# Performance work log

Hardware: AMD Instinct MI355X
Metric: run time of the kernel (lower is better)

The kernel has to match this reference:

```python
import jax, jax.numpy as jnp
import numpy as np

FILLER = 10.1  # filler_value from __init__
B, C, L, KEEP = 128, 16, 16384, 12288


def setup_inputs() -> dict:
    key = jax.random.key(0)
    k1, k2, k3, k4 = jax.random.split(key, 4)
    x1 = jax.random.normal(k1, (B, C, 4096), dtype=jnp.float32)
    x2 = jax.random.normal(k2, (B, C, 4096), dtype=jnp.float32)
    x3 = jax.random.normal(k3, (B, C, L), dtype=jnp.float32)
    # Scatter exactly (L - KEEP) filler entries at random positions in every row,
    # so per-row compaction yields a uniform length KEEP (required by np.stack
    # in the original module).
    u = jax.random.uniform(k4, (B, C, L))
    ranks = jnp.argsort(jnp.argsort(u, axis=-1), axis=-1)  # random permutation ranks
    fill_mask = ranks < (L - KEEP)
    x3 = jnp.where(fill_mask, jnp.float32(FILLER), x3)
    return {"x1": x1, "x2": x2, "x3": x3, "keep_len": KEEP}


def reference(x1, x2, x3, keep_len):
    # Per-row stream compaction: drop entries equal to FILLER, keep original
    # order of survivors, output fixed length keep_len.
    is_filler = x3 == jnp.float32(FILLER)          # [B, C, L] bool
    # Stable argsort moves non-filler (False=0) to the front, order-preserving.
    order = jnp.argsort(is_filler, axis=-1, stable=True)  # [B, C, L]
    compacted = jnp.take_along_axis(x3, order, axis=-1)    # [B, C, L]
    return compacted[..., :keep_len]                        # [B, C, keep_len]
```

## Files before the change

kernel.cpp:

```cpp
#include <hip/hip_runtime.h>


#define FILLER_VAL 10.1f
constexpr int L_LEN = 16384;
constexpr int KEEP_LEN = 12288;
constexpr int BLOCK = 256;
constexpr int CHUNK = BLOCK * 4;

__global__ __launch_bounds__(BLOCK) void compact_rows_kernel(
    const float* __restrict__ x3, float* __restrict__ out)
{
    const int row = blockIdx.x;
    const float* __restrict__ in = x3 + (size_t)row * L_LEN;
    float* __restrict__ o = out + (size_t)row * KEEP_LEN;

    const int tid  = threadIdx.x;
    const int lane = tid & 63;
    const int wid  = tid >> 6;

    __shared__ int wave_tot[BLOCK / 64];

    const unsigned long long lt_mask = (1ULL << lane) - 1ULL;

    int base = 0;

    #pragma unroll 1
    for (int chunk = 0; chunk < L_LEN; chunk += CHUNK) {
        float4 v = *reinterpret_cast<const float4*>(in + chunk + tid * 4);

        const bool p0 = v.x != FILLER_VAL;
        const bool p1 = v.y != FILLER_VAL;
        const bool p2 = v.z != FILLER_VAL;
        const bool p3 = v.w != FILLER_VAL;

        const unsigned long long m0 = __ballot(p0);
        const unsigned long long m1 = __ballot(p1);
        const unsigned long long m2 = __ballot(p2);
        const unsigned long long m3 = __ballot(p3);

        const int before = __popcll(m0 & lt_mask) + __popcll(m1 & lt_mask)
                         + __popcll(m2 & lt_mask) + __popcll(m3 & lt_mask);
        const int wtot   = __popcll(m0) + __popcll(m1) + __popcll(m2) + __popcll(m3);

        if (lane == 0) wave_tot[wid] = wtot;
        __syncthreads();

        int wave_base = 0;
        #pragma unroll
        for (int w = 0; w < BLOCK / 64; ++w) {
            if (w < wid) wave_base += wave_tot[w];
        }
        int chunk_total = 0;
        #pragma unroll
        for (int w = 0; w < BLOCK / 64; ++w) chunk_total += wave_tot[w];

        int pos = base + wave_base + before;

        if (p0) { if (pos < KEEP_LEN) o[pos] = v.x; ++pos; }
        if (p1) { if (pos < KEEP_LEN) o[pos] = v.y; ++pos; }
        if (p2) { if (pos < KEEP_LEN) o[pos] = v.z; ++pos; }
        if (p3) { if (pos < KEEP_LEN) o[pos] = v.w; ++pos; }

        base += chunk_total;
        __syncthreads();
    }
}

extern "C" void kernel_launch(void* const* d_in, const int* in_sizes, int n_in,
                              void* d_out, int out_size, void* d_ws, size_t ws_size,
                              hipStream_t stream)
{
    const float* x3 = (const float*)d_in[2];
    float* out = (float*)d_out;

    const int rows = in_sizes[2] / L_LEN;

    compact_rows_kernel<<<rows, BLOCK, 0, stream>>>(x3, out);
}
```

Before: 262.0 us.

## Load whole row into registers upfront and batch wave-count syncs per half

The loop of sixteen chunks, each with its own global load and two barriers, is replaced by issuing all sixteen float4 loads per thread up front, held in two register arrays of eight chunks. Ballots and wave totals are computed for eight chunks at a time and stored in a shared table, so a whole half needs only one barrier. This targets load latency and barrier stalls in a kernel that runs one block per row. In exchange, register use per thread rises sharply, which may lower occupancy.

```diff
diff --git a/kernel.cpp b/kernel.cpp
--- a/kernel.cpp
+++ b/kernel.cpp
@@ -2,10 +2,12 @@
 
 
 #define FILLER_VAL 10.1f
-constexpr int L_LEN = 16384;
+constexpr int L_LEN   = 16384;
 constexpr int KEEP_LEN = 12288;
-constexpr int BLOCK = 256;
-constexpr int CHUNK = BLOCK * 4;
+constexpr int BLOCK   = 256;
+constexpr int NW      = BLOCK / 64;
+constexpr int CHUNK   = BLOCK * 4;
+constexpr int HC      = 8;
 
 __global__ __launch_bounds__(BLOCK) void compact_rows_kernel(
     const float* __restrict__ x3, float* __restrict__ out)
@@ -17,52 +19,81 @@
     const int tid  = threadIdx.x;
     const int lane = tid & 63;
     const int wid  = tid >> 6;
+    const unsigned long long lt = (1ULL << lane) - 1ULL;
 
-    __shared__ int wave_tot[BLOCK / 64];
+    __shared__ int wtot[2][HC][NW];
 
-    const unsigned long long lt_mask = (1ULL << lane) - 1ULL;
+    float4 va[HC], vb[HC];
+    #pragma unroll
+    for (int c = 0; c < HC; ++c)
+        va[c] = *reinterpret_cast<const float4*>(in + c * CHUNK + tid * 4);
+    #pragma unroll
+    for (int c = 0; c < HC; ++c)
+        vb[c] = *reinterpret_cast<const float4*>(in + (HC + c) * CHUNK + tid * 4);
 
-    int base = 0;
+    int before_a[HC];
+    #pragma unroll
+    for (int c = 0; c < HC; ++c) {
+        unsigned long long m0 = __ballot(va[c].x != FILLER_VAL);
+        unsigned long long m1 = __ballot(va[c].y != FILLER_VAL);
+        unsigned long long m2 = __ballot(va[c].z != FILLER_VAL);
+        unsigned long long m3 = __ballot(va[c].w != FILLER_VAL);
+        before_a[c] = __popcll(m0 & lt) + __popcll(m1 & lt)
+                    + __popcll(m2 & lt) + __popcll(m3 & lt);
+        if (lane == 0)
+            wtot[0][c][wid] = __popcll(m0) + __popcll(m1)
+                            + __popcll(m2) + __popcll(m3);
+    }
+    __syncthreads();
 
-    #pragma unroll 1
-    for (int chunk = 0; chunk < L_LEN; chunk += CHUNK) {
-        float4 v = *reinterpret_cast<const float4*>(in + chunk + tid * 4);
+    int run = 0;
+    #pragma unroll
+    for (int c = 0; c < HC; ++c) {
+        int wb = run;
+        #pragma unroll
+        for (int w = 0; w < NW; ++w) {
+            int t = wtot[0][c][w];
+            if (w < wid) wb += t;
+            run += t;
+        }
+        int pos = wb + before_a[c];
+        float4 v = va[c];
+        if (v.x != FILLER_VAL) { if (pos < KEEP_LEN) o[pos] = v.x; ++pos; }
+        if (v.y != FILLER_VAL) { if (pos < KEEP_LEN) o[pos] = v.y; ++pos; }
+        if (v.z != FILLER_VAL) { if (pos < KEEP_LEN) o[pos] = v.z; ++pos; }
+        if (v.w != FILLER_VAL) { if (pos < KEEP_LEN) o[pos] = v.w; ++pos; }
+    }
 
-        const bool p0 = v.x != FILLER_VAL;
-        const bool p1 = v.y != FILLER_VAL;
-        const bool p2 = v.z != FILLER_VAL;
-        const bool p3 = v.w != FILLER_VAL;
+    int before_b[HC];
+    #pragma unroll
+    for (int c = 0; c < HC; ++c) {
+        unsigned long long m0 = __ballot(vb[c].x != FILLER_VAL);
+        unsigned long long m1 = __ballot(vb[c].y != FILLER_VAL);
+        unsigned long long m2 = __ballot(vb[c].z != FILLER_VAL);
+        unsigned long long m3 = __ballot(vb[c].w != FILLER_VAL);
+        before_b[c] = __popcll(m0 & lt) + __popcll(m1 & lt)
+                    + __popcll(m2 & lt) + __popcll(m3 & lt);
+        if (lane == 0)
+            wtot[1][c][wid] = __popcll(m0) + __popcll(m1)
+                            + __popcll(m2) + __popcll(m3);
+    }
+    __syncthreads();
 
-        const unsigned long long m0 = __ballot(p0);
-        const unsigned long long m1 = __ballot(p1);
-        const unsigned long long m2 = __ballot(p2);
-        const unsigned long long m3 = __ballot(p3);
-
-        const int before = __popcll(m0 & lt_mask) + __popcll(m1 & lt_mask)
-                         + __popcll(m2 & lt_mask) + __popcll(m3 & lt_mask);
-        const int wtot   = __popcll(m0) + __popcll(m1) + __popcll(m2) + __popcll(m3);
-
-        if (lane == 0) wave_tot[wid] = wtot;
-        __syncthreads();
-
-        int wave_base = 0;
+    #pragma unroll
+    for (int c = 0; c < HC; ++c) {
+        int wb = run;
         #pragma unroll
-        for (int w = 0; w < BLOCK / 64; ++w) {
-            if (w < wid) wave_base += wave_tot[w];
+        for (int w = 0; w < NW; ++w) {
+            int t = wtot[1][c][w];
+            if (w < wid) wb += t;
+            run += t;
         }
-        int chunk_total = 0;
-        #pragma unroll
-        for (int w = 0; w < BLOCK / 64; ++w) chunk_total += wave_tot[w];
-
-        int pos = base + wave_base + before;
-
-        if (p0) { if (pos < KEEP_LEN) o[pos] = v.x; ++pos; }
-        if (p1) { if (pos < KEEP_LEN) o[pos] = v.y; ++pos; }
-        if (p2) { if (pos < KEEP_LEN) o[pos] = v.z; ++pos; }
-        if (p3) { if (pos < KEEP_LEN) o[pos] = v.w; ++pos; }
-
-        base += chunk_total;
-        __syncthreads();
+        int pos = wb + before_b[c];
+        float4 v = vb[c];
+        if (v.x != FILLER_VAL) { if (pos < KEEP_LEN) o[pos] = v.x; ++pos; }
+        if (v.y != FILLER_VAL) { if (pos < KEEP_LEN) o[pos] = v.y; ++pos; }
+        if (v.z != FILLER_VAL) { if (pos < KEEP_LEN) o[pos] = v.z; ++pos; }
+        if (v.w != FILLER_VAL) { if (pos < KEEP_LEN) o[pos] = v.w; ++pos; }
     }
 }
 
```

Result: no change. 259.0 us (-1.2%).

## Load whole row into registers, compact via LDS staging, write coalesced float4

Applied to the files above, without the earlier changes.

Each block now issues all 16 float4 loads for its row up front, computes every chunk's ballot and prefix in one pass with a single barrier, and scatters survivors into a 48KB LDS staging buffer. The buffer is then written to global memory with coalesced float4 stores instead of scattered 4-byte stores. The aim is to remove the per-chunk barriers and the serial load latency, and to make the writes fully coalesced. In exchange it uses 64 float registers for the row plus 48KB of LDS per block, which limits occupancy. The output is only fully written when the row has at least KEEP_LEN survivors, which holds for the test inputs.

```diff
diff --git a/kernel.cpp b/kernel.cpp
--- a/kernel.cpp
+++ b/kernel.cpp
@@ -2,10 +2,12 @@
 
 
 #define FILLER_VAL 10.1f
-constexpr int L_LEN = 16384;
+constexpr int L_LEN    = 16384;
 constexpr int KEEP_LEN = 12288;
-constexpr int BLOCK = 256;
-constexpr int CHUNK = BLOCK * 4;
+constexpr int BLOCK    = 256;
+constexpr int NW       = BLOCK / 64;
+constexpr int CHUNK    = BLOCK * 4;
+constexpr int NC       = L_LEN / CHUNK;
 
 __global__ __launch_bounds__(BLOCK) void compact_rows_kernel(
     const float* __restrict__ x3, float* __restrict__ out)
@@ -17,52 +19,54 @@
     const int tid  = threadIdx.x;
     const int lane = tid & 63;
     const int wid  = tid >> 6;
+    const unsigned long long lt = (1ULL << lane) - 1ULL;
 
-    __shared__ int wave_tot[BLOCK / 64];
+    __shared__ float stage[KEEP_LEN];
+    __shared__ int wtot[NC][NW];
 
-    const unsigned long long lt_mask = (1ULL << lane) - 1ULL;
+    float4 v[NC];
+    #pragma unroll
+    for (int c = 0; c < NC; ++c)
+        v[c] = *reinterpret_cast<const float4*>(in + c * CHUNK + tid * 4);
 
-    int base = 0;
+    int before[NC];
+    #pragma unroll
+    for (int c = 0; c < NC; ++c) {
+        unsigned long long m0 = __ballot(v[c].x != FILLER_VAL);
+        unsigned long long m1 = __ballot(v[c].y != FILLER_VAL);
+        unsigned long long m2 = __ballot(v[c].z != FILLER_VAL);
+        unsigned long long m3 = __ballot(v[c].w != FILLER_VAL);
+        before[c] = __popcll(m0 & lt) + __popcll(m1 & lt)
+                  + __popcll(m2 & lt) + __popcll(m3 & lt);
+        if (lane == 0)
+            wtot[c][wid] = __popcll(m0) + __popcll(m1)
+                         + __popcll(m2) + __popcll(m3);
+    }
+    __syncthreads();
 
-    #pragma unroll 1
-    for (int chunk = 0; chunk < L_LEN; chunk += CHUNK) {
-        float4 v = *reinterpret_cast<const float4*>(in + chunk + tid * 4);
+    int run = 0;
+    #pragma unroll
+    for (int c = 0; c < NC; ++c) {
+        int wb = run;
+        #pragma unroll
+        for (int w = 0; w < NW; ++w) {
+            int t = wtot[c][w];
+            if (w < wid) wb += t;
+            run += t;
+        }
+        int pos = wb + before[c];
+        if (v[c].x != FILLER_VAL) { if (pos < KEEP_LEN) stage[pos] = v[c].x; ++pos; }
+        if (v[c].y != FILLER_VAL) { if (pos < KEEP_LEN) stage[pos] = v[c].y; ++pos; }
+        if (v[c].z != FILLER_VAL) { if (pos < KEEP_LEN) stage[pos] = v[c].z; ++pos; }
+        if (v[c].w != FILLER_VAL) { if (pos < KEEP_LEN) stage[pos] = v[c].w; ++pos; }
+    }
+    __syncthreads();
 
-        const bool p0 = v.x != FILLER_VAL;
-        const bool p1 = v.y != FILLER_VAL;
-        const bool p2 = v.z != FILLER_VAL;
-        const bool p3 = v.w != FILLER_VAL;
-
-        const unsigned long long m0 = __ballot(p0);
-        const unsigned long long m1 = __ballot(p1);
-        const unsigned long long m2 = __ballot(p2);
-        const unsigned long long m3 = __ballot(p3);
-
-        const int before = __popcll(m0 & lt_mask) + __popcll(m1 & lt_mask)
-                         + __popcll(m2 & lt_mask) + __popcll(m3 & lt_mask);
-        const int wtot   = __popcll(m0) + __popcll(m1) + __popcll(m2) + __popcll(m3);
-
-        if (lane == 0) wave_tot[wid] = wtot;
-        __syncthreads();
-
-        int wave_base = 0;
-        #pragma unroll
-        for (int w = 0; w < BLOCK / 64; ++w) {
-            if (w < wid) wave_base += wave_tot[w];
-        }
-        int chunk_total = 0;
-        #pragma unroll
-        for (int w = 0; w < BLOCK / 64; ++w) chunk_total += wave_tot[w];
-
-        int pos = base + wave_base + before;
-
-        if (p0) { if (pos < KEEP_LEN) o[pos] = v.x; ++pos; }
-        if (p1) { if (pos < KEEP_LEN) o[pos] = v.y; ++pos; }
-        if (p2) { if (pos < KEEP_LEN) o[pos] = v.z; ++pos; }
-        if (p3) { if (pos < KEEP_LEN) o[pos] = v.w; ++pos; }
-
-        base += chunk_total;
-        __syncthreads();
+    #pragma unroll
+    for (int k = 0; k < KEEP_LEN / (BLOCK * 4); ++k) {
+        const int idx = (k * BLOCK + tid) * 4;
+        float4 val = *reinterpret_cast<const float4*>(&stage[idx]);
+        *reinterpret_cast<float4*>(&o[idx]) = val;
     }
 }
 
```

New measurement: 256.5 us. 1.02x faster.
